# Kernel tuning notes

Hardware: AMD Instinct MI355X
Metric: run time of the kernel (lower is better)

The kernel has to match this reference:

```python
import jax, jax.numpy as jnp
import numpy as np

BATCH = 2048
DIM = 4096
TEMPERATURE = 0.5
KD_T = 1.0
KD_WEIGHT = 1.0


def setup_inputs() -> dict:
    key = jax.random.key(0)
    k1, k2 = jax.random.split(key)
    emb_target = jax.random.normal(k1, (BATCH, DIM), dtype=jnp.float32)
    emb_surrogate = jax.random.normal(k2, (BATCH, DIM), dtype=jnp.float32)
    return {"emb_target": emb_target, "emb_surrogate": emb_surrogate}


def reference(emb_target, emb_surrogate):
    B = emb_target.shape[0]
    # --- NT-Xent contrastive loss ---
    reps = jnp.concatenate([emb_target, emb_surrogate], axis=0)  # [2B, D]
    # cosine similarity via normalized matmul (eps matches torch cosine_similarity clamp)
    norms = jnp.maximum(jnp.linalg.norm(reps, axis=1, keepdims=True), 1e-8)
    z = reps / norms
    sim = z @ z.T  # [2B, 2B]
    idx = jnp.arange(2 * B)
    # positives: diag offsets +B and -B -> sim[i, (i+B) mod 2B]
    positives = sim[idx, (idx + B) % (2 * B)]  # [2B]
    nominator = jnp.exp(positives / TEMPERATURE)
    neg_mask = 1.0 - jnp.eye(2 * B, dtype=sim.dtype)
    denominator = jnp.sum(neg_mask * jnp.exp(sim / TEMPERATURE), axis=1)  # [2B]
    cont_loss = jnp.sum(-jnp.log(nominator / denominator)) / (2 * B)
    # --- KD softmax-KL ---
    soft_targets = jax.nn.softmax(emb_target / KD_T, axis=-1)
    soft_prob = jax.nn.log_softmax(emb_surrogate / KD_T, axis=-1)
    kd_loss = jnp.sum(soft_targets * (jnp.log(soft_targets) - soft_prob)) / B * KD_T ** 2
    # --- MSE ---
    mse = jnp.mean((emb_surrogate - emb_target) ** 2)
    return cont_loss + KD_WEIGHT * kd_loss + mse
```

## Files before the change

### kernel.cpp

```cpp
#include <hip/hip_runtime.h>
#include <hip/hip_bf16.h>

#define TWO_B 4096
#define DIM_ 4096

typedef __attribute__((ext_vector_type(8))) short bf16x8;
typedef __attribute__((ext_vector_type(4))) float f32x4;
typedef __attribute__((ext_vector_type(4))) int i32x4;
typedef __attribute__((ext_vector_type(8))) int i32x8;

static __device__ __forceinline__ unsigned short f2bf(float x) {
    return __builtin_bit_cast(unsigned short, __float2bfloat16(x));
}

static __device__ __forceinline__ float waveReduceSum(float v) {
    v += __shfl_xor(v, 1);  v += __shfl_xor(v, 2);  v += __shfl_xor(v, 4);
    v += __shfl_xor(v, 8);  v += __shfl_xor(v, 16); v += __shfl_xor(v, 32);
    return v;
}
static __device__ __forceinline__ float waveReduceMax(float v) {
    v = fmaxf(v, __shfl_xor(v, 1));  v = fmaxf(v, __shfl_xor(v, 2));
    v = fmaxf(v, __shfl_xor(v, 4));  v = fmaxf(v, __shfl_xor(v, 8));
    v = fmaxf(v, __shfl_xor(v, 16)); v = fmaxf(v, __shfl_xor(v, 32));
    return v;
}

static __device__ __forceinline__ int enc_fp4(float q) {
    float a = fabsf(q);
    int m = a < 0.25f ? 0 : a < 0.75f ? 1 : a < 1.25f ? 2 : a < 1.75f ? 3 :
            a < 2.5f  ? 4 : a < 3.5f  ? 5 : a < 5.0f  ? 6 : 7;
    return m | (q < 0.f ? 8 : 0);
}

__global__ __launch_bounds__(256) void row_stats(
    const float* __restrict__ et, const float* __restrict__ es,
    float* __restrict__ rinv, float* __restrict__ qs,
    float* __restrict__ kdp, float* __restrict__ msep,
    float* __restrict__ rowsum, char* __restrict__ z4)
{
    const int b = blockIdx.x;
    const int tid = threadIdx.x;
    const int wid = tid >> 6;

    if (b < 16) rowsum[b * 256 + tid] = 0.f;

    const float4* tp = (const float4*)(et + (size_t)b * DIM_);
    const float4* sp = (const float4*)(es + (size_t)b * DIM_);
    float4 tv[4], sv[4];
#pragma unroll
    for (int i = 0; i < 4; ++i) { tv[i] = tp[tid * 4 + i]; sv[i] = sp[tid * 4 + i]; }

    float mt = -1e30f, ms = -1e30f, amt = 0.f, ams = 0.f;
    float nt2 = 0.f, ns2 = 0.f, msev = 0.f;
#pragma unroll
    for (int i = 0; i < 4; ++i) {
        const float* tx = (const float*)&tv[i];
        const float* sx = (const float*)&sv[i];
#pragma unroll
        for (int j = 0; j < 4; ++j) {
            float a = tx[j], c = sx[j];
            mt = fmaxf(mt, a); ms = fmaxf(ms, c);
            amt = fmaxf(amt, fabsf(a)); ams = fmaxf(ams, fabsf(c));
            nt2 += a * a; ns2 += c * c;
            float d = c - a; msev += d * d;
        }
    }
    mt = waveReduceMax(mt); ms = waveReduceMax(ms);
    amt = waveReduceMax(amt); ams = waveReduceMax(ams);
    __shared__ float smx[4], sms[4], sat[4], sas[4];
    if ((tid & 63) == 0) { smx[wid] = mt; sms[wid] = ms; sat[wid] = amt; sas[wid] = ams; }
    __syncthreads();
    mt = fmaxf(fmaxf(smx[0], smx[1]), fmaxf(smx[2], smx[3]));
    ms = fmaxf(fmaxf(sms[0], sms[1]), fmaxf(sms[2], sms[3]));
    const float maT = fmaxf(fmaxf(fmaxf(sat[0], sat[1]), fmaxf(sat[2], sat[3])), 1e-20f);
    const float maS = fmaxf(fmaxf(fmaxf(sas[0], sas[1]), fmaxf(sas[2], sas[3])), 1e-20f);

    float se_t = 0.f, st = 0.f, sx_ = 0.f, se_s = 0.f;
#pragma unroll
    for (int i = 0; i < 4; ++i) {
        const float* tx = (const float*)&tv[i];
        const float* sx = (const float*)&sv[i];
#pragma unroll
        for (int j = 0; j < 4; ++j) {
            float a = tx[j], c = sx[j];
            float e = __expf(a - mt);
            se_t += e; st += e * a; sx_ += e * c;
            se_s += __expf(c - ms);
        }
    }
    float v0 = waveReduceSum(se_t), v1 = waveReduceSum(st), v2 = waveReduceSum(sx_);
    float v3 = waveReduceSum(se_s), v4 = waveReduceSum(nt2), v5 = waveReduceSum(ns2);
    float v6 = waveReduceSum(msev);
    __shared__ float sred[7][4];
    if ((tid & 63) == 0) {
        sred[0][wid] = v0; sred[1][wid] = v1; sred[2][wid] = v2; sred[3][wid] = v3;
        sred[4][wid] = v4; sred[5][wid] = v5; sred[6][wid] = v6;
    }
    __syncthreads();
    const float rT = sred[4][0] + sred[4][1] + sred[4][2] + sred[4][3];
    const float rS = sred[5][0] + sred[5][1] + sred[5][2] + sred[5][3];
    const float rinvT = 1.f / fmaxf(sqrtf(rT), 1e-8f);
    const float rinvS = 1.f / fmaxf(sqrtf(rS), 1e-8f);

    if (tid == 0) {
        float r0 = sred[0][0] + sred[0][1] + sred[0][2] + sred[0][3];
        float r1 = sred[1][0] + sred[1][1] + sred[1][2] + sred[1][3];
        float r2 = sred[2][0] + sred[2][1] + sred[2][2] + sred[2][3];
        float r3 = sred[3][0] + sred[3][1] + sred[3][2] + sred[3][3];
        float r6 = sred[6][0] + sred[6][1] + sred[6][2] + sred[6][3];
        float lse_t = mt + logf(r0);
        float lse_s = ms + logf(r3);
        kdp[b]  = (r1 - r2) / r0 - lse_t + lse_s;
        msep[b] = r6;
        rinv[b]        = rinvT;
        rinv[b + 2048] = rinvS;
        qs[b]          = maT * rinvT * (1.f / 6.f);
        qs[b + 2048]   = maS * rinvS * (1.f / 6.f);
    }

    if (z4) {
        const float gT = 6.f / maT, gS = 6.f / maS;
        int wt[2] = {0, 0}, wsv[2] = {0, 0};
#pragma unroll
        for (int i = 0; i < 4; ++i) {
            const float* tx = (const float*)&tv[i];
            const float* sx = (const float*)&sv[i];
            int bt = (enc_fp4(tx[0] * gT)) | (enc_fp4(tx[1] * gT) << 4) |
                     (enc_fp4(tx[2] * gT) << 8) | (enc_fp4(tx[3] * gT) << 12);
            int bs = (enc_fp4(sx[0] * gS)) | (enc_fp4(sx[1] * gS) << 4) |
                     (enc_fp4(sx[2] * gS) << 8) | (enc_fp4(sx[3] * gS) << 12);
            wt[i >> 1] |= bt << (16 * (i & 1));
            wsv[i >> 1] |= bs << (16 * (i & 1));
        }
        ((int2*)(z4 + (size_t)b * 2048))[tid] = make_int2(wt[0], wt[1]);
        ((int2*)(z4 + (size_t)(b + 2048) * 2048))[tid] = make_int2(wsv[0], wsv[1]);
    }
}

__global__ __launch_bounds__(256, 2) void cont_gemm_fp4(
    const char* __restrict__ z4, const float* __restrict__ qs,
    float* __restrict__ rowsum, float* __restrict__ pos)
{
    const int bid = blockIdx.x;
    int t = (bid & 7) * 66 + (bid >> 3);
    int bi = 0;
    while (t >= (32 - bi)) { t -= (32 - bi); ++bi; }
    const int bj = bi + t;
    const int brow = bi * 128, bcol = bj * 128;
    const bool dg = (bi == bj);

    __shared__ char As[128 * 128];
    __shared__ char Bs[128 * 128];

    const int tid = threadIdx.x;
    const int lane = tid & 63;
    const int wid = tid >> 6;
    const int wm = wid >> 1, wn = wid & 1;
    const int lrow = lane >> 3;
    const int lblk = lane & 7;

    const char* srcA[4];
    const char* srcB[4];
#pragma unroll
    for (int i = 0; i < 4; ++i) {
        int r = wid * 32 + i * 8 + lrow;
        srcA[i] = z4 + (size_t)(brow + r) * 2048 + ((lblk ^ lrow) << 4);
        srcB[i] = z4 + (size_t)(bcol + r) * 2048 + ((lblk ^ lrow) << 4);
    }

    const char* Bbase = dg ? As : Bs;
    const int sc1 = 0x7F7F7F7F;

    f32x4 acc[4][4] = {};

    for (int ktb = 0; ktb < 2048; ktb += 128) {
        __syncthreads();
#pragma unroll
        for (int i = 0; i < 4; ++i) {
            char* dstA = As + (wid * 32 + i * 8) * 128;
            __builtin_amdgcn_global_load_lds(
                (const __attribute__((address_space(1))) unsigned int*)(srcA[i] + ktb),
                (__attribute__((address_space(3))) unsigned int*)dstA, 16, 0, 0);
        }
        if (!dg) {
#pragma unroll
            for (int i = 0; i < 4; ++i) {
                char* dstB = Bs + (wid * 32 + i * 8) * 128;
                __builtin_amdgcn_global_load_lds(
                    (const __attribute__((address_space(1))) unsigned int*)(srcB[i] + ktb),
                    (__attribute__((address_space(3))) unsigned int*)dstB, 16, 0, 0);
            }
        }
        __syncthreads();
#pragma unroll
        for (int ks = 0; ks < 2; ++ks) {
            i32x4 af4[4], bf4[4];
            const int li = lane & 15;
            const int kb = ks * 64 + (lane >> 4) * 16;
#pragma unroll
            for (int m = 0; m < 4; ++m) {
                int r = wm * 64 + m * 16 + li;
                int off = (r * 128 + kb) ^ ((r & 7) << 4);
                af4[m] = *(const i32x4*)(As + off);
            }
#pragma unroll
            for (int n = 0; n < 4; ++n) {
                int r = wn * 64 + n * 16 + li;
                int off = (r * 128 + kb) ^ ((r & 7) << 4);
                bf4[n] = *(const i32x4*)(Bbase + off);
            }
            __builtin_amdgcn_s_setprio(1);
#pragma unroll
            for (int m = 0; m < 4; ++m) {
                i32x8 a8 = {af4[m][0], af4[m][1], af4[m][2], af4[m][3], 0, 0, 0, 0};
#pragma unroll
                for (int n = 0; n < 4; ++n) {
                    i32x8 b8 = {bf4[n][0], bf4[n][1], bf4[n][2], bf4[n][3], 0, 0, 0, 0};
                    acc[m][n] = __builtin_amdgcn_mfma_scale_f32_16x16x128_f8f6f4(
                        a8, b8, acc[m][n], 4, 4, 0, sc1, 0, sc1);
                }
            }
            __builtin_amdgcn_s_setprio(0);
        }
    }

    const bool posT = (bj == bi + 16);
    const int li = lane & 15;
    const int lg = lane >> 4;
    float sB[4];
#pragma unroll
    for (int n = 0; n < 4; ++n) sB[n] = qs[bcol + wn * 64 + n * 16 + li];
    float cs[4] = {0.f, 0.f, 0.f, 0.f};
#pragma unroll
    for (int m = 0; m < 4; ++m) {
#pragma unroll
        for (int q = 0; q < 4; ++q) {
            int lr = wm * 64 + m * 16 + lg * 4 + q;
            int gr = brow + lr;
            float sA = qs[gr];
            float rsum = 0.f;
#pragma unroll
            for (int n = 0; n < 4; ++n) {
                int gc = bcol + wn * 64 + n * 16 + li;
                float v = acc[m][n][q] * sA * sB[n];
                if (posT && gc == gr + 2048) { pos[gr] = v; pos[gc] = v; }
                float e = (dg && gr == gc) ? 0.f : __expf(2.0f * v);
                rsum += e;
                cs[n] += e;
            }
            rsum += __shfl_xor(rsum, 1);
            rsum += __shfl_xor(rsum, 2);
            rsum += __shfl_xor(rsum, 4);
            rsum += __shfl_xor(rsum, 8);
            if (li == 0) atomicAdd(&rowsum[gr], rsum);
        }
    }
    if (!dg) {
#pragma unroll
        for (int n = 0; n < 4; ++n) {
            float v = cs[n];
            v += __shfl_xor(v, 16);
            v += __shfl_xor(v, 32);
            if (lg == 0) atomicAdd(&rowsum[bcol + wn * 64 + n * 16 + li], v);
        }
    }
}

__global__ __launch_bounds__(256) void cont_gemm(
    const float* __restrict__ et, const float* __restrict__ es,
    const float* __restrict__ rinv, float* __restrict__ rowsum,
    float* __restrict__ pos)
{
    int t = blockIdx.x;
    int bi = 0;
    while (t >= (32 - bi)) { t -= (32 - bi); ++bi; }
    const int bj = bi + t;
    const int brow = bi * 128, bcol = bj * 128;

    __shared__ unsigned short As[128 * 64];
    __shared__ unsigned short Bs[128 * 64];

    const int tid = threadIdx.x;
    const int lane = tid & 63;
    const int wid = tid >> 6;
    const int wm = wid >> 1, wn = wid & 1;

    const int srow = tid >> 4;
    const int sf4 = tid & 15;

    const float* pA[8]; const float* pB[8];
    float riA[8], riB[8];
#pragma unroll
    for (int it = 0; it < 8; ++it) {
        int r = srow + it * 16;
        int ga = brow + r;
        int gb = bcol + r;
        pA[it] = (ga < 2048) ? (et + (size_t)ga * DIM_) : (es + (size_t)(ga - 2048) * DIM_);
        pB[it] = (gb < 2048) ? (et + (size_t)gb * DIM_) : (es + (size_t)(gb - 2048) * DIM_);
        riA[it] = rinv[ga]; riB[it] = rinv[gb];
    }

    f32x4 acc[4][4] = {};

    for (int kt = 0; kt < DIM_; kt += 64) {
        __syncthreads();
#pragma unroll
        for (int it = 0; it < 8; ++it) {
            int r = srow + it * 16;
            int swz = (r & 7) << 4;
            int bo = (r * 128 + sf4 * 8) ^ swz;
            {
                float4 v = *(const float4*)(pA[it] + kt + sf4 * 4);
                float ri = riA[it];
                ushort4 pk = make_ushort4(f2bf(v.x * ri), f2bf(v.y * ri),
                                          f2bf(v.z * ri), f2bf(v.w * ri));
                *(ushort4*)((char*)As + bo) = pk;
            }
            {
                float4 v = *(const float4*)(pB[it] + kt + sf4 * 4);
                float ri = riB[it];
                ushort4 pk = make_ushort4(f2bf(v.x * ri), f2bf(v.y * ri),
                                          f2bf(v.z * ri), f2bf(v.w * ri));
                *(ushort4*)((char*)Bs + bo) = pk;
            }
        }
        __syncthreads();
#pragma unroll
        for (int ks = 0; ks < 2; ++ks) {
            bf16x8 af[4], bfr[4];
            const int li = lane & 15;
            const int kb = ks * 64 + (lane >> 4) * 16;
#pragma unroll
            for (int m = 0; m < 4; ++m) {
                int r = wm * 64 + m * 16 + li;
                int off = (r * 128 + kb) ^ ((r & 7) << 4);
                af[m] = *(const bf16x8*)((const char*)As + off);
            }
#pragma unroll
            for (int n = 0; n < 4; ++n) {
                int r = wn * 64 + n * 16 + li;
                int off = (r * 128 + kb) ^ ((r & 7) << 4);
                bfr[n] = *(const bf16x8*)((const char*)Bs + off);
            }
#pragma unroll
            for (int m = 0; m < 4; ++m)
#pragma unroll
                for (int n = 0; n < 4; ++n)
                    acc[m][n] = __builtin_amdgcn_mfma_f32_16x16x32_bf16(
                        af[m], bfr[n], acc[m][n], 0, 0, 0);
        }
    }

    const bool diag = (bi == bj);
    const bool posT = (bcol == (brow ^ 2048));
    const int li = lane & 15;
    const int lg = lane >> 4;
    float cs[4] = {0.f, 0.f, 0.f, 0.f};
#pragma unroll
    for (int m = 0; m < 4; ++m) {
#pragma unroll
        for (int q = 0; q < 4; ++q) {
            int lr = wm * 64 + m * 16 + lg * 4 + q;
            float rsum = 0.f;
#pragma unroll
            for (int n = 0; n < 4; ++n) {
                int lc = wn * 64 + n * 16 + li;
                float v = acc[m][n][q];
                if (posT && lc == lr) { pos[brow + lr] = v; pos[bcol + lc] = v; }
                float e = (diag && lc == lr) ? 0.f : __expf(2.0f * v);
                rsum += e;
                cs[n] += e;
            }
            rsum += __shfl_xor(rsum, 1);
            rsum += __shfl_xor(rsum, 2);
            rsum += __shfl_xor(rsum, 4);
            rsum += __shfl_xor(rsum, 8);
            if (li == 0) atomicAdd(&rowsum[brow + lr], rsum);
        }
    }
    if (!diag) {
#pragma unroll
        for (int n = 0; n < 4; ++n) {
            float v = cs[n];
            v += __shfl_xor(v, 16);
            v += __shfl_xor(v, 32);
            if (lg == 0) atomicAdd(&rowsum[bcol + wn * 64 + n * 16 + li], v);
        }
    }
}

__global__ __launch_bounds__(256) void finalize(
    const float* __restrict__ rowsum, const float* __restrict__ pos,
    const float* __restrict__ kdp, const float* __restrict__ msep,
    float* __restrict__ out)
{
    const int tid = threadIdx.x;
    float c = 0.f;
    for (int i = tid; i < TWO_B; i += 256)
        c += logf(rowsum[i]) - 2.0f * pos[i];
    float kd = 0.f, ms = 0.f;
    for (int i = tid; i < 2048; i += 256) { kd += kdp[i]; ms += msep[i]; }
    c = waveReduceSum(c); kd = waveReduceSum(kd); ms = waveReduceSum(ms);
    __shared__ float sm[3][4];
    if ((tid & 63) == 0) { sm[0][tid >> 6] = c; sm[1][tid >> 6] = kd; sm[2][tid >> 6] = ms; }
    __syncthreads();
    if (tid == 0) {
        float cont = (sm[0][0] + sm[0][1] + sm[0][2] + sm[0][3]) / 4096.0f;
        float kds  = (sm[1][0] + sm[1][1] + sm[1][2] + sm[1][3]) / 2048.0f;
        float mses = (sm[2][0] + sm[2][1] + sm[2][2] + sm[2][3]) / (2048.0f * 4096.0f);
        out[0] = cont + kds + mses;
    }
}

extern "C" void kernel_launch(void* const* d_in, const int* in_sizes, int n_in,
                              void* d_out, int out_size, void* d_ws, size_t ws_size,
                              hipStream_t stream) {
    const float* et = (const float*)d_in[0];
    const float* es = (const float*)d_in[1];

    const size_t Z_BYTES = (size_t)TWO_B * 2048;
    const size_t SMALL_FLOATS = 4096 * 4 + 2048 * 2;
    const bool fast = ws_size >= Z_BYTES + SMALL_FLOATS * sizeof(float);

    if (fast) {
        char* z4 = (char*)d_ws;
        float* smallf = (float*)((char*)d_ws + Z_BYTES);
        float* rowsum = smallf;
        float* pos  = smallf + 4096;
        float* qs   = smallf + 4096 * 2;
        float* rinv = smallf + 4096 * 3;
        float* kdp  = smallf + 4096 * 4;
        float* msep = smallf + 4096 * 4 + 2048;
        hipLaunchKernelGGL(row_stats, dim3(2048), dim3(256), 0, stream,
                           et, es, rinv, qs, kdp, msep, rowsum, z4);
        hipLaunchKernelGGL(cont_gemm_fp4, dim3(528), dim3(256), 0, stream, z4, qs, rowsum, pos);
        hipLaunchKernelGGL(finalize, dim3(1), dim3(256), 0, stream, rowsum, pos, kdp, msep, (float*)d_out);
    } else {
        float* ws = (float*)d_ws;
        float* rowsum = ws;
        float* pos  = ws + 4096;
        float* qs   = ws + 4096 * 2;
        float* rinv = ws + 4096 * 3;
        float* kdp  = ws + 4096 * 4;
        float* msep = ws + 4096 * 4 + 2048;
        hipMemsetAsync(rowsum, 0, 4096 * sizeof(float), stream);
        hipLaunchKernelGGL(row_stats, dim3(2048), dim3(256), 0, stream,
                           et, es, rinv, qs, kdp, msep, rowsum, (char*)nullptr);
        hipLaunchKernelGGL(cont_gemm, dim3(528), dim3(256), 0, stream, et, es, rinv, rowsum, pos);
        hipLaunchKernelGGL(finalize, dim3(1), dim3(256), 0, stream, rowsum, pos, kdp, msep, (float*)d_out);
    }
}
```

Measured before the change: 65.90 us.

## Double-buffer FP4 GEMM LDS tiles to overlap global loads with MFMA

The FP4 contrastive GEMM now uses two LDS buffers for the A and B tiles. The next K-tile is prefetched with global_load_lds while the current one is computed, and explicit vmcnt waits plus s_barrier replace the two __syncthreads per iteration. This is meant to hide global-memory latency behind MFMA work. It doubles LDS usage per block, which could affect occupancy, and relies on hand-counted vmcnt values being correct.

```diff
diff --git a/kernel.cpp b/kernel.cpp
--- a/kernel.cpp
+++ b/kernel.cpp
@@ -137,7 +137,7 @@
     }
 }
 
-__global__ __launch_bounds__(256, 2) void cont_gemm_fp4(
+__global__ __launch_bounds__(256, 2) void cont_gemm_fp4db(
     const char* __restrict__ z4, const float* __restrict__ qs,
     float* __restrict__ rowsum, float* __restrict__ pos)
 {
@@ -149,8 +149,8 @@
     const int brow = bi * 128, bcol = bj * 128;
     const bool dg = (bi == bj);
 
-    __shared__ char As[128 * 128];
-    __shared__ char Bs[128 * 128];
+    __shared__ char As[2][128 * 128];
+    __shared__ char Bs[2][128 * 128];
 
     const int tid = threadIdx.x;
     const int lane = tid & 63;
@@ -168,16 +168,15 @@
         srcB[i] = z4 + (size_t)(bcol + r) * 2048 + ((lblk ^ lrow) << 4);
     }
 
-    const char* Bbase = dg ? As : Bs;
     const int sc1 = 0x7F7F7F7F;
 
     f32x4 acc[4][4] = {};
 
-    for (int ktb = 0; ktb < 2048; ktb += 128) {
-        __syncthreads();
+    auto STAGE = [&](int buf, int step) {
+        const int ktb = step * 128;
 #pragma unroll
         for (int i = 0; i < 4; ++i) {
-            char* dstA = As + (wid * 32 + i * 8) * 128;
+            char* dstA = &As[buf][(wid * 32 + i * 8) * 128];
             __builtin_amdgcn_global_load_lds(
                 (const __attribute__((address_space(1))) unsigned int*)(srcA[i] + ktb),
                 (__attribute__((address_space(3))) unsigned int*)dstA, 16, 0, 0);
@@ -185,29 +184,33 @@
         if (!dg) {
 #pragma unroll
             for (int i = 0; i < 4; ++i) {
-                char* dstB = Bs + (wid * 32 + i * 8) * 128;
+                char* dstB = &Bs[buf][(wid * 32 + i * 8) * 128];
                 __builtin_amdgcn_global_load_lds(
                     (const __attribute__((address_space(1))) unsigned int*)(srcB[i] + ktb),
                     (__attribute__((address_space(3))) unsigned int*)dstB, 16, 0, 0);
             }
         }
-        __syncthreads();
+    };
+
+    auto COMPUTE = [&](int buf) {
+        const char* Ab = &As[buf][0];
+        const char* Bb = dg ? &As[buf][0] : &Bs[buf][0];
+        const int li = lane & 15;
 #pragma unroll
         for (int ks = 0; ks < 2; ++ks) {
             i32x4 af4[4], bf4[4];
-            const int li = lane & 15;
             const int kb = ks * 64 + (lane >> 4) * 16;
 #pragma unroll
             for (int m = 0; m < 4; ++m) {
                 int r = wm * 64 + m * 16 + li;
                 int off = (r * 128 + kb) ^ ((r & 7) << 4);
-                af4[m] = *(const i32x4*)(As + off);
+                af4[m] = *(const i32x4*)(Ab + off);
             }
 #pragma unroll
             for (int n = 0; n < 4; ++n) {
                 int r = wn * 64 + n * 16 + li;
                 int off = (r * 128 + kb) ^ ((r & 7) << 4);
-                bf4[n] = *(const i32x4*)(Bbase + off);
+                bf4[n] = *(const i32x4*)(Bb + off);
             }
             __builtin_amdgcn_s_setprio(1);
 #pragma unroll
@@ -222,7 +225,40 @@
             }
             __builtin_amdgcn_s_setprio(0);
         }
-    }
+    };
+
+    auto WAIT_TILE = [&](bool last) {
+        if (last) {
+            asm volatile("s_waitcnt vmcnt(0)" ::: "memory");
+        } else if (dg) {
+            asm volatile("s_waitcnt vmcnt(4)" ::: "memory");
+        } else {
+            asm volatile("s_waitcnt vmcnt(8)" ::: "memory");
+        }
+    };
+
+    STAGE(0, 0);
+    STAGE(1, 1);
+
+    for (int tt = 0; tt < 14; tt += 2) {
+        WAIT_TILE(false);
+        __builtin_amdgcn_s_barrier();
+        COMPUTE(0);
+        __builtin_amdgcn_s_barrier();
+        STAGE(0, tt + 2);
+        WAIT_TILE(false);
+        __builtin_amdgcn_s_barrier();
+        COMPUTE(1);
+        __builtin_amdgcn_s_barrier();
+        STAGE(1, tt + 3);
+    }
+    WAIT_TILE(false);
+    __builtin_amdgcn_s_barrier();
+    COMPUTE(0);
+    __builtin_amdgcn_s_barrier();
+    WAIT_TILE(true);
+    __builtin_amdgcn_s_barrier();
+    COMPUTE(1);
 
     const bool posT = (bj == bi + 16);
     const int li = lane & 15;
@@ -433,7 +469,7 @@
         float* msep = smallf + 4096 * 4 + 2048;
         hipLaunchKernelGGL(row_stats, dim3(2048), dim3(256), 0, stream,
                            et, es, rinv, qs, kdp, msep, rowsum, z4);
-        hipLaunchKernelGGL(cont_gemm_fp4, dim3(528), dim3(256), 0, stream, z4, qs, rowsum, pos);
+        hipLaunchKernelGGL(cont_gemm_fp4db, dim3(528), dim3(256), 0, stream, z4, qs, rowsum, pos);
         hipLaunchKernelGGL(finalize, dim3(1), dim3(256), 0, stream, rowsum, pos, kdp, msep, (float*)d_out);
     } else {
         float* ws = (float*)d_ws;
```

After: 79.52 us. 1.21x slower.
